# Kernel optimization log

Measured on AMD Instinct MI355X. Metric: run time of the kernel, lower is better.

Reference implementation:

```python
import jax, jax.numpy as jnp
import numpy as np

NUM_ITERATIONS = 3


def _squash_elementwise(s):
    # Faithful to original: squared_norm summed over trailing axis of size 1
    # => elementwise squash v = s^2 * s / ((1 + s^2) * sqrt(s^2))
    sq = s * s
    return sq * s / ((1.0 + sq) * jnp.sqrt(sq))


def setup_inputs() -> dict:
    key = jax.random.key(0)
    k1, k2 = jax.random.split(key)
    B, R, C, O, I = 256, 1152, 10, 16, 8
    x = jax.random.normal(k1, (B, R, I), dtype=jnp.float32)
    W = jax.random.normal(k2, (R, C, O, I), dtype=jnp.float32)
    return {"x": x, "W": W}


def reference(x, W):
    # x: (B, R, I); W: (R, C, O, I)
    R, C, O, I = W.shape
    # u_hat[b,r,c,o] = sum_i W[r,c,o,i] * x[b,r,i]   (matmul W @ x per route/capsule)
    u_hat = jnp.einsum('rcoi,bri->brco', W, x)  # (B, R, C, O)
    b_ij = jnp.zeros((R, C), dtype=x.dtype)  # batch-shared routing logits
    v = None
    for it in range(NUM_ITERATIONS):
        c_ij = jax.nn.softmax(b_ij, axis=0)  # softmax over routes (dim=1 in torch)
        s_j = jnp.einsum('rc,brco->bco', c_ij, u_hat)  # weighted sum over routes
        v = _squash_elementwise(s_j)  # (B, C, O)
        if it < NUM_ITERATIONS - 1:
            # agreement a[b,r,c] = u_hat[b,r,c,:] . v[b,c,:]
            a_ij = jnp.einsum('brco,bco->brc', u_hat, v)
            b_ij = b_ij + a_ij.mean(axis=0)  # mean over batch, batch-shared update
    return v[..., None]  # (B, C, O, 1) matches v_j.squeeze(1)
```

## Files before the change

kernel.cpp:

```cpp
#include <hip/hip_runtime.h>

static constexpr int B_ = 256;
static constexpr int R_ = 1152;
static constexpr int C_ = 10;
static constexpr int O_ = 16;
static constexpr int I_ = 8;
static constexpr int SCO = C_ * O_;
static constexpr int K_ = R_ * I_;
static constexpr int NB = 256;

typedef short bf16x8 __attribute__((ext_vector_type(8)));
typedef float f32x4  __attribute__((ext_vector_type(4)));

__device__ __forceinline__ unsigned short f2bf(float f) {
  union { float f; unsigned int u; } c; c.f = f;
  const unsigned int u = c.u;
  return (unsigned short)((u + 0x7fffu + ((u >> 16) & 1u)) >> 16);
}
__device__ __forceinline__ float bf2f(unsigned short h) {
  union { unsigned int u; float f; } c; c.u = ((unsigned int)h) << 16; return c.f;
}

__device__ __forceinline__ void gsync(unsigned int* bar, unsigned int epoch) {
  __syncthreads();
  if (threadIdx.x == 0)
    __hip_atomic_store(&bar[blockIdx.x * 16], epoch,
                       __ATOMIC_RELEASE, __HIP_MEMORY_SCOPE_AGENT);
  if (blockIdx.x == 0) {
    if (threadIdx.x < 256) {
      int guard = 0;
      while (__hip_atomic_load(&bar[threadIdx.x * 16],
                               __ATOMIC_RELAXED, __HIP_MEMORY_SCOPE_AGENT) < epoch) {
        __builtin_amdgcn_s_sleep(8);
        if (++guard > (1 << 17)) break;
      }
    }
    __syncthreads();
    if (threadIdx.x < 8)
      __hip_atomic_store(&bar[4096 + threadIdx.x * 16], epoch,
                         __ATOMIC_RELEASE, __HIP_MEMORY_SCOPE_AGENT);
  } else {
    if (threadIdx.x == 0) {
      unsigned int* g = &bar[4096 + (blockIdx.x & 7) * 16];
      int guard = 0;
      while (__hip_atomic_load(g, __ATOMIC_RELAXED,
                               __HIP_MEMORY_SCOPE_AGENT) < epoch) {
        __builtin_amdgcn_s_sleep(32);
        if (++guard > (1 << 16)) break;
      }
    }
  }
  __syncthreads();
  asm volatile("" ::: "memory");
}

__device__ __forceinline__ void gemm_phase(
    int git, const unsigned short* __restrict__ xb,
    const unsigned short* __restrict__ wraw, const float* __restrict__ eX,
    float* __restrict__ Z, unsigned short* __restrict__ vbw,
    float* __restrict__ out, unsigned char* smem,
    int bx, int t, int w, int mrow, int quad) {
  float* sred = (float*)smem;
  float* szed = (float*)(smem + 16384);
  float* e_lds = (float*)(smem + 20480);
  const int xcd = bx & 7, j = bx >> 3;
  const int mtile = (xcd >> 1) * 4 + j / 5;
  const int c = (xcd & 1) * 5 + j % 5;
  const int m0 = mtile * 16;
  if (git > 0) {
    for (int idx = t; idx < 1152; idx += 512) e_lds[idx] = eX[c * 1152 + idx];
    if (t < 10) szed[t] = atomicAdd(&Z[git * 10 + t], 0.0f);
    __syncthreads();
  }
  const unsigned short* ap = xb + (size_t)(m0 + mrow) * K_ + w * 1152 + quad * 8;
  const unsigned short* bp = wraw + ((size_t)(w * 144 + quad) * C_ + c) * 128 + mrow * 8;
  f32x4 acc = {0.0f, 0.0f, 0.0f, 0.0f};
  if (git == 0) {
#pragma unroll 6
    for (int kk = 0; kk < 36; ++kk) {
      const bf16x8 a = *(const bf16x8*)(ap + kk * 32);
      const bf16x8 b = *(const bf16x8*)(bp + (size_t)kk * 5120);
      acc = __builtin_amdgcn_mfma_f32_16x16x32_bf16(a, b, acc, 0, 0, 0);
    }
  } else {
#pragma unroll 6
    for (int kk = 0; kk < 36; ++kk) {
      const bf16x8 a = *(const bf16x8*)(ap + kk * 32);
      const bf16x8 braw = *(const bf16x8*)(bp + (size_t)kk * 5120);
      const float ev = e_lds[w * 144 + kk * 4 + quad];
      bf16x8 b;
#pragma unroll
      for (int j8 = 0; j8 < 8; ++j8)
        b[j8] = (short)f2bf(bf2f((unsigned short)braw[j8]) * ev);
      acc = __builtin_amdgcn_mfma_f32_16x16x32_bf16(a, b, acc, 0, 0, 0);
    }
  }
#pragma unroll
  for (int rg = 0; rg < 4; ++rg)
    sred[w * 272 + mrow * 17 + quad * 4 + rg] = acc[rg];
  __syncthreads();
  if (t < 256) {
    int m, n;
    if (git == 2) { m = t >> 4; n = t & 15; } else { n = t >> 4; m = t & 15; }
    const int e = n * 17 + m;
    const float ss = ((sred[0 * 272 + e] + sred[1 * 272 + e]) +
                      (sred[2 * 272 + e] + sred[3 * 272 + e])) +
                     ((sred[4 * 272 + e] + sred[5 * 272 + e]) +
                      (sred[6 * 272 + e] + sred[7 * 272 + e]));
    const float s = (git == 0) ? ss * (1.0f / 1152.0f) : ss / szed[c];
    const float v = s * fabsf(s) / (1.0f + s * s);
    if (git == 2) out[(size_t)(m0 + m) * SCO + c * 16 + n] = v;
    else          vbw[(size_t)(c * 16 + n) * 256 + m0 + m] = f2bf(v);
  }
}

__device__ __forceinline__ void pv_phase(
    int it, const unsigned short* __restrict__ xT,
    const unsigned short* __restrict__ vbr, const float* __restrict__ W,
    const unsigned short* __restrict__ wraw_unused,
    float* __restrict__ bvec, float* __restrict__ eOut, float* __restrict__ Z,
    unsigned char* smem, int bx, int t, int lane, int w, int mrow, int quad) {
  unsigned short* svb = (unsigned short*)smem;
  float* sp = (float*)smem;
  float* sbs = (float*)(smem + 81920);
  const int seg = (bx & 7) * 18 + (bx >> 3);
  const int r0 = seg * 8;
  bf16x8 afr[8];
  if (w < 4) {
    const unsigned short* ap = xT + (size_t)(seg * 64 + w * 16 + mrow) * 256 + quad * 8;
#pragma unroll
    for (int kk = 0; kk < 8; ++kk) afr[kk] = *(const bf16x8*)(ap + kk * 32);
  }
  {
    const char* src = (const char*)vbr;
    char* dst = (char*)svb;
#pragma unroll
    for (int i = 0; i < 10; ++i) {
      const int ci = i * 512 + t;
      const int lin = ci * 16;
      const int n = ci >> 5;
      *(bf16x8*)(dst + (lin ^ ((n & 7) << 4))) = *(const bf16x8*)(src + lin);
    }
  }
  __syncthreads();
  f32x4 acc[10];
  if (w < 4) {
#pragma unroll
    for (int c = 0; c < 10; ++c) acc[c] = (f32x4){0.0f, 0.0f, 0.0f, 0.0f};
#pragma unroll
    for (int c = 0; c < 10; ++c) {
      const int n = c * 16 + mrow;
      const int base = n * 512 + quad * 16;
#pragma unroll
      for (int kk = 0; kk < 8; ++kk) {
        const bf16x8 b = *(const bf16x8*)((const char*)svb +
                          ((base + kk * 64) ^ ((n & 7) << 4)));
        acc[c] = __builtin_amdgcn_mfma_f32_16x16x32_bf16(afr[kk], b, acc[c], 0, 0, 0);
      }
    }
  }
  __syncthreads();
  if (w < 4) {
#pragma unroll
    for (int c = 0; c < 10; ++c)
#pragma unroll
      for (int rg = 0; rg < 4; ++rg) {
        const int ml = w * 16 + quad * 4 + rg;
        sp[(c * 8 + (ml >> 3)) * 128 + mrow * 8 + (ml & 7)] = acc[c][rg];
      }
  }
  __syncthreads();
  const int p16 = t >> 5, l32 = t & 31;
#pragma unroll
  for (int ch = 0; ch < 5; ++ch) {
    const int pair = ch * 16 + p16;
    const int rl = pair / 10, c = pair - rl * 10;
    const float4 pv4 = *(const float4*)&sp[(c * 8 + rl) * 128 + l32 * 4];
    const float4 wv = *(const float4*)(W + (size_t)(r0 + rl) * 1280 + c * 128 + l32 * 4);
    float prod = wv.x * pv4.x + wv.y * pv4.y + wv.z * pv4.z + wv.w * pv4.w;
    prod += __shfl_xor(prod, 1);  prod += __shfl_xor(prod, 2);
    prod += __shfl_xor(prod, 4);  prod += __shfl_xor(prod, 8);
    prod += __shfl_xor(prod, 16);
    if (l32 == 0) sbs[rl * 10 + c] = prod;
  }
  __syncthreads();
  if (t < 80) {
    const int rl = t / 10, c = t - rl * 10;
    const int r = r0 + rl;
    float b = sbs[t] * (1.0f / 256.0f);
    if (it != 0) b += bvec[r * C_ + c];
    bvec[r * C_ + c] = b;
    const float e = expf(b);
    sbs[t] = e;
    eOut[c * 1152 + r] = e;
  }
  __syncthreads();
  if (t < 10) {
    float z = 0.0f;
#pragma unroll
    for (int rl = 0; rl < 8; ++rl) z += sbs[rl * 10 + t];
    atomicAdd(&Z[(it + 1) * 10 + t], z);
  }
}

__global__ __launch_bounds__(512, 1) void mega(
    const float* __restrict__ x, const float* __restrict__ W,
    float* __restrict__ out, unsigned int* __restrict__ bar,
    float* __restrict__ bvec, float* __restrict__ Z,
    float* __restrict__ eA, float* __restrict__ eB,
    unsigned short* __restrict__ xb, unsigned short* __restrict__ wraw,
    unsigned short* __restrict__ xT,
    unsigned short* __restrict__ vb0, unsigned short* __restrict__ vb1) {
  __shared__ __align__(16) unsigned char smem[82560];
  const int bx = blockIdx.x;
  const int t = threadIdx.x;
  const int lane = t & 63;
  const int w = __builtin_amdgcn_readfirstlane(t >> 6);
  const int mrow = lane & 15, quad = lane >> 4;

  {
    const float4* wf = (const float4*)W;
    ushort4* wr = (ushort4*)wraw;
    for (int idx = t; idx < 1440; idx += 512) {
      const int j = bx * 1440 + idx;
      const float4 v4 = wf[j];
      ushort4 r4;
      r4.x = f2bf(v4.x); r4.y = f2bf(v4.y); r4.z = f2bf(v4.z); r4.w = f2bf(v4.w);
      wr[j] = r4;
    }
    if (bx == 0 && t < 32) Z[t] = 0.0f;
    float* sx = (float*)smem;
    const int bq = bx & 3, rseg = bx >> 2;
    const int rbase = rseg * 18;
    for (int idx = t; idx < 64 * 36; idx += 512) {
      const int b = idx / 36, f4 = idx - b * 36;
      const size_t off = (size_t)(bq * 64 + b) * K_ + rbase * I_ + f4 * 4;
      const float4 val = *(const float4*)(x + off);
      ushort4 o4;
      o4.x = f2bf(val.x); o4.y = f2bf(val.y); o4.z = f2bf(val.z); o4.w = f2bf(val.w);
      *(ushort4*)(xb + off) = o4;
      const int rr = f4 >> 1, i4 = (f4 & 1) * 4;
      sx[(rr * 8 + i4 + 0) * 68 + b] = val.x;
      sx[(rr * 8 + i4 + 1) * 68 + b] = val.y;
      sx[(rr * 8 + i4 + 2) * 68 + b] = val.z;
      sx[(rr * 8 + i4 + 3) * 68 + b] = val.w;
    }
    __syncthreads();
    for (int row = w * 18; row < w * 18 + 18; ++row)
      xT[(size_t)(rseg * 144 + row) * 256 + bq * 64 + lane] = f2bf(sx[row * 68 + lane]);
  }
  gsync(bar, 1);

  if (bx < 160) gemm_phase(0, xb, wraw, nullptr, Z, vb0, out, smem, bx, t, w, mrow, quad);
  gsync(bar, 2);

  if (bx < 144) pv_phase(0, xT, vb0, W, wraw, bvec, eA, Z, smem, bx, t, lane, w, mrow, quad);
  gsync(bar, 3);

  if (bx < 160) gemm_phase(1, xb, wraw, eA, Z, vb1, out, smem, bx, t, w, mrow, quad);
  gsync(bar, 4);

  if (bx < 144) pv_phase(1, xT, vb1, W, wraw, bvec, eB, Z, smem, bx, t, lane, w, mrow, quad);
  gsync(bar, 5);

  if (bx < 160) gemm_phase(2, xb, wraw, eB, Z, nullptr, out, smem, bx, t, w, mrow, quad);
}

extern "C" void kernel_launch(void* const* d_in, const int* in_sizes, int n_in,
                              void* d_out, int out_size, void* d_ws, size_t ws_size,
                              hipStream_t stream) {
  const float* x = (const float*)d_in[0];
  const float* W = (const float*)d_in[1];
  float* out = (float*)d_out;

  unsigned int* bar = (unsigned int*)d_ws;
  float* bvec = (float*)d_ws + 4224;
  float* Z    = bvec + R_ * C_;
  float* eA   = Z + 32;
  float* eB   = eA + C_ * R_;
  unsigned short* xb   = (unsigned short*)(eB + C_ * R_);
  unsigned short* wraw = xb + (size_t)B_ * K_;
  unsigned short* xT   = wraw + (size_t)R_ * C_ * O_ * I_;
  unsigned short* vb0  = xT + (size_t)R_ * 8 * 256;
  unsigned short* vb1  = vb0 + (size_t)160 * 256;

  hipMemsetAsync(bar, 0, 16896, stream);
  mega<<<NB, 512, 0, stream>>>(x, W, out, bar, bvec, Z, eA, eB,
                               xb, wraw, xT, vb0, vb1);
}
```

Baseline: 150.5 us.

## Rework grid barrier with per-XCD request/ack handshake before release

Replaces the grid barrier's gather-then-broadcast with a multi-step protocol. Block 0 gathers arrival flags and posts per-group requests. Each block reads its hardware XCC_ID and counts itself into a per-XCD response counter, and the first arrival per XCD bumps an ack counter. Block 0 waits for acks from every populated XCD before issuing a release fence and the go flags. The intent appears to be ensuring cross-XCD visibility or cache ordering with fewer release operations, and spin sleep intervals are shortened. The cost is extra atomic round trips per barrier, a larger workspace region to clear, and reliance on XCC_ID register semantics.

```diff
diff --git a/kernel.cpp b/kernel.cpp
--- a/kernel.cpp
+++ b/kernel.cpp
@@ -21,32 +21,76 @@
   union { unsigned int u; float f; } c; c.u = ((unsigned int)h) << 16; return c.f;
 }
 
-__device__ __forceinline__ void gsync(unsigned int* bar, unsigned int epoch) {
-  __syncthreads();
-  if (threadIdx.x == 0)
-    __hip_atomic_store(&bar[blockIdx.x * 16], epoch,
-                       __ATOMIC_RELEASE, __HIP_MEMORY_SCOPE_AGENT);
-  if (blockIdx.x == 0) {
-    if (threadIdx.x < 256) {
+#define FLAG_IDX(b)    ((b) * 16)
+#define REQ_IDX(k)     (4096 + (k) * 16)
+#define ACK_IDX(e)     (4224 + ((e) - 1) * 16)
+#define GO_IDX(k)      (4352 + (k) * 16)
+#define RESP_IDX(e, x) (4480 + (((e) - 1) * 8 + (x)) * 16)
+#define NBLK_IDX(x)    (5120 + (x) * 16)
+
+__device__ __forceinline__ void gsync(unsigned int* bar, unsigned int epoch,
+                                      unsigned int myxcd) {
+  __syncthreads();
+  const int bx = blockIdx.x, t = threadIdx.x;
+  if (bx == 0) {
+    if (t == 0)
+      __hip_atomic_store(&bar[FLAG_IDX(0)], epoch,
+                         __ATOMIC_RELAXED, __HIP_MEMORY_SCOPE_AGENT);
+    if (t < 256) {
       int guard = 0;
-      while (__hip_atomic_load(&bar[threadIdx.x * 16],
+      while (__hip_atomic_load(&bar[FLAG_IDX(t)],
                                __ATOMIC_RELAXED, __HIP_MEMORY_SCOPE_AGENT) < epoch) {
+        __builtin_amdgcn_s_sleep(4);
+        if (++guard > (1 << 18)) break;
+      }
+    }
+    __syncthreads();
+    if (t == 0) {
+      for (int k2 = 0; k2 < 8; ++k2)
+        __hip_atomic_store(&bar[REQ_IDX(k2)], epoch,
+                           __ATOMIC_RELAXED, __HIP_MEMORY_SCOPE_AGENT);
+      const unsigned oldr = __hip_atomic_fetch_add(&bar[RESP_IDX(epoch, myxcd)], 1u,
+                              __ATOMIC_RELAXED, __HIP_MEMORY_SCOPE_AGENT);
+      if (oldr == 0)
+        __hip_atomic_fetch_add(&bar[ACK_IDX(epoch)], 1u,
+                               __ATOMIC_RELEASE, __HIP_MEMORY_SCOPE_AGENT);
+      unsigned nx = 0;
+      for (int x2 = 0; x2 < 8; ++x2)
+        nx += (__hip_atomic_load(&bar[NBLK_IDX(x2)],
+                 __ATOMIC_RELAXED, __HIP_MEMORY_SCOPE_AGENT) > 0u) ? 1u : 0u;
+      int guard = 0;
+      while (__hip_atomic_load(&bar[ACK_IDX(epoch)],
+                               __ATOMIC_RELAXED, __HIP_MEMORY_SCOPE_AGENT) < nx) {
+        __builtin_amdgcn_s_sleep(4);
+        if (++guard > (1 << 18)) break;
+      }
+      __builtin_amdgcn_fence(__ATOMIC_RELEASE, "agent");
+      for (int k2 = 0; k2 < 8; ++k2)
+        __hip_atomic_store(&bar[GO_IDX(k2)], epoch,
+                           __ATOMIC_RELAXED, __HIP_MEMORY_SCOPE_AGENT);
+    }
+  } else {
+    if (t == 0) {
+      __hip_atomic_store(&bar[FLAG_IDX(bx)], epoch,
+                         __ATOMIC_RELAXED, __HIP_MEMORY_SCOPE_AGENT);
+      unsigned int* rq = &bar[REQ_IDX(bx & 7)];
+      int guard = 0;
+      while (__hip_atomic_load(rq, __ATOMIC_RELAXED,
+                               __HIP_MEMORY_SCOPE_AGENT) < epoch) {
         __builtin_amdgcn_s_sleep(8);
         if (++guard > (1 << 17)) break;
       }
-    }
-    __syncthreads();
-    if (threadIdx.x < 8)
-      __hip_atomic_store(&bar[4096 + threadIdx.x * 16], epoch,
-                         __ATOMIC_RELEASE, __HIP_MEMORY_SCOPE_AGENT);
-  } else {
-    if (threadIdx.x == 0) {
-      unsigned int* g = &bar[4096 + (blockIdx.x & 7) * 16];
-      int guard = 0;
+      const unsigned oldr = __hip_atomic_fetch_add(&bar[RESP_IDX(epoch, myxcd)], 1u,
+                              __ATOMIC_RELAXED, __HIP_MEMORY_SCOPE_AGENT);
+      if (oldr == 0)
+        __hip_atomic_fetch_add(&bar[ACK_IDX(epoch)], 1u,
+                               __ATOMIC_RELEASE, __HIP_MEMORY_SCOPE_AGENT);
+      unsigned int* g = &bar[GO_IDX(bx & 7)];
+      guard = 0;
       while (__hip_atomic_load(g, __ATOMIC_RELAXED,
                                __HIP_MEMORY_SCOPE_AGENT) < epoch) {
-        __builtin_amdgcn_s_sleep(32);
-        if (++guard > (1 << 16)) break;
+        __builtin_amdgcn_s_sleep(16);
+        if (++guard > (1 << 17)) break;
       }
     }
   }
@@ -117,9 +161,8 @@
 __device__ __forceinline__ void pv_phase(
     int it, const unsigned short* __restrict__ xT,
     const unsigned short* __restrict__ vbr, const float* __restrict__ W,
-    const unsigned short* __restrict__ wraw_unused,
     float* __restrict__ bvec, float* __restrict__ eOut, float* __restrict__ Z,
-    unsigned char* smem, int bx, int t, int lane, int w, int mrow, int quad) {
+    unsigned char* smem, int bx, int t, int w, int mrow, int quad) {
   unsigned short* svb = (unsigned short*)smem;
   float* sp = (float*)smem;
   float* sbs = (float*)(smem + 81920);
@@ -218,6 +261,14 @@
   const int w = __builtin_amdgcn_readfirstlane(t >> 6);
   const int mrow = lane & 15, quad = lane >> 4;
 
+  unsigned int myxcd;
+  asm volatile("s_getreg_b32 %0, hwreg(HW_REG_XCC_ID)" : "=s"(myxcd));
+  myxcd &= 7u;
+  if (t == 0)
+    __hip_atomic_fetch_add(&bar[NBLK_IDX(myxcd)], 1u,
+                           __ATOMIC_RELAXED, __HIP_MEMORY_SCOPE_AGENT);
+  if (bx == 0 && t < 32) Z[t] = 0.0f;
+
   {
     const float4* wf = (const float4*)W;
     ushort4* wr = (ushort4*)wraw;
@@ -228,7 +279,6 @@
       r4.x = f2bf(v4.x); r4.y = f2bf(v4.y); r4.z = f2bf(v4.z); r4.w = f2bf(v4.w);
       wr[j] = r4;
     }
-    if (bx == 0 && t < 32) Z[t] = 0.0f;
     float* sx = (float*)smem;
     const int bq = bx & 3, rseg = bx >> 2;
     const int rbase = rseg * 18;
@@ -249,19 +299,19 @@
     for (int row = w * 18; row < w * 18 + 18; ++row)
       xT[(size_t)(rseg * 144 + row) * 256 + bq * 64 + lane] = f2bf(sx[row * 68 + lane]);
   }
-  gsync(bar, 1);
+  gsync(bar, 1, myxcd);
 
   if (bx < 160) gemm_phase(0, xb, wraw, nullptr, Z, vb0, out, smem, bx, t, w, mrow, quad);
-  gsync(bar, 2);
-
-  if (bx < 144) pv_phase(0, xT, vb0, W, wraw, bvec, eA, Z, smem, bx, t, lane, w, mrow, quad);
-  gsync(bar, 3);
+  gsync(bar, 2, myxcd);
+
+  if (bx < 144) pv_phase(0, xT, vb0, W, bvec, eA, Z, smem, bx, t, w, mrow, quad);
+  gsync(bar, 3, myxcd);
 
   if (bx < 160) gemm_phase(1, xb, wraw, eA, Z, vb1, out, smem, bx, t, w, mrow, quad);
-  gsync(bar, 4);
-
-  if (bx < 144) pv_phase(1, xT, vb1, W, wraw, bvec, eB, Z, smem, bx, t, lane, w, mrow, quad);
-  gsync(bar, 5);
+  gsync(bar, 4, myxcd);
+
+  if (bx < 144) pv_phase(1, xT, vb1, W, bvec, eB, Z, smem, bx, t, w, mrow, quad);
+  gsync(bar, 5, myxcd);
 
   if (bx < 160) gemm_phase(2, xb, wraw, eB, Z, nullptr, out, smem, bx, t, w, mrow, quad);
 }
@@ -274,7 +324,7 @@
   float* out = (float*)d_out;
 
   unsigned int* bar = (unsigned int*)d_ws;
-  float* bvec = (float*)d_ws + 4224;
+  float* bvec = (float*)d_ws + 5376;
   float* Z    = bvec + R_ * C_;
   float* eA   = Z + 32;
   float* eB   = eA + C_ * R_;
@@ -284,7 +334,7 @@
   unsigned short* vb0  = xT + (size_t)R_ * 8 * 256;
   unsigned short* vb1  = vb0 + (size_t)160 * 256;
 
-  hipMemsetAsync(bar, 0, 16896, stream);
+  hipMemsetAsync(bar, 0, 21504, stream);
   mega<<<NB, 512, 0, stream>>>(x, W, out, bar, bvec, Z, eA, eB,
                                xb, wraw, xT, vb0, vb1);
 }
```

Measured after the change: 136.9 us. 1.1x faster.
